# Kernel tuning notes

Measured on AMD Instinct MI355X. Metric: run time of the kernel, lower is better.

## Reference

```python
import jax, jax.numpy as jnp
import numpy as np

N_INP, N_INN, N_STEP = 512, 256, 3


def _linear(x, W, b):
    # torch nn.Linear convention: y = x @ W.T + b, W: (out, in)
    return x @ W.T + b


def _outer_linear(fv, W, b):
    # Linear(2h -> out) applied to outer_concat(fv) without materializing the 2h concat.
    # out[b,i,j] = fv[b,i] @ W[:, :h].T + fv[b,j] @ W[:, h:].T + b
    h = fv.shape[-1]
    x = fv @ W[:, :h].T  # (b, l, out)
    y = fv @ W[:, h:].T  # (b, l, out)
    return x[:, :, None, :] + y[:, None, :, :] + b  # (b, l, l, out)


def setup_inputs() -> dict:
    key = jax.random.key(0)
    ks = jax.random.split(key, 16)
    b, l = 8, 128
    s_inp = 1.0 / np.sqrt(N_INP)
    s_inn = 1.0 / np.sqrt(N_INN)
    s_2in = 1.0 / np.sqrt(2 * N_INN)
    u = lambda k, shape, s: jax.random.uniform(k, shape, jnp.float32, -s, s)
    return {
        "feat": jax.random.normal(ks[0], (b, l, N_INP), jnp.float32),
        "mask": jnp.ones((b, l), jnp.float32),
        "W_inp": u(ks[1], (N_INN, N_INP), s_inp), "b_inp": u(ks[2], (N_INN,), s_inp),
        "W_oup": u(ks[3], (N_INP, N_INN), s_inn), "b_oup": u(ks[4], (N_INP,), s_inn),
        "W_fe": u(ks[5], (N_INN, 2 * N_INN), s_2in), "b_fe": u(ks[6], (N_INN,), s_2in),
        "W_ue": u(ks[7], (N_INN, 2 * N_INN), s_2in), "b_ue": u(ks[8], (N_INN,), s_2in),
        "W_agg": u(ks[9], (N_INN, N_INN), s_inn), "b_agg": u(ks[10], (N_INN,), s_inn),
        "W_uv": u(ks[11], (N_INN, 2 * N_INN), s_2in), "b_uv": u(ks[12], (N_INN,), s_2in),
        "W_attn": u(ks[13], (N_INN, N_INN), s_inn), "b_attn": u(ks[14], (N_INN,), s_inn),
    }


def reference(feat, mask, W_inp, b_inp, W_oup, b_oup, W_fe, b_fe, W_ue, b_ue,
              W_agg, b_agg, W_uv, b_uv, W_attn, b_attn):
    h = N_INN
    fv = _linear(feat, W_inp, b_inp)                 # (b, l, h)
    fe = _outer_linear(fv, W_fe, b_fe)               # (b, l, l, h)
    for _ in range(N_STEP):
        # edge_update: xform_feat_e(outer_concat(fv)) then upd_e(concat(., fe))
        new_e = _outer_linear(fv, W_fe, b_fe)        # (b, l, l, h)
        fe = new_e @ W_ue[:, :h].T + fe @ W_ue[:, h:].T + b_ue
        # vertex_update (vectorized over j; softmax over source index i = dim 1)
        hid = fv * mask[:, :, None]
        xhid = _linear(hid, W_agg, b_agg)            # (b, l, h)
        attn = _linear(fe, W_attn, b_attn)           # (b, i, j, h)
        w = jax.nn.softmax(attn, axis=1)             # softmax over i
        agg = jax.nn.sigmoid(jnp.einsum('bijh,bih->bjh', w, xhid))  # (b, l, h)
        fv = _linear(jnp.concatenate([xhid, agg], axis=2), W_uv, b_uv)  # dropout = identity (eval)
    return _linear(fv, W_oup, b_oup)                 # (b, l, n_inp)
```

## Files before the change

kernel.cpp:

```cpp
#include <hip/hip_runtime.h>
#include <math.h>


typedef float f32x4  __attribute__((ext_vector_type(4)));
typedef short bf16x8 __attribute__((ext_vector_type(8)));

#define H  256
#define H2 512

__device__ __forceinline__ ushort f2bf(float f) {
    uint u = __float_as_uint(f);
    u += 0x7FFFu + ((u >> 16) & 1u);
    return (ushort)(u >> 16);
}
__device__ __forceinline__ float bf2f(ushort h) {
    return __uint_as_float(((uint)h) << 16);
}

struct Args {
    const float *feat, *mask, *b_inp, *b_oup, *b_agg, *b_uv;
    const float *W_fe, *W_inp, *W_oup, *W_ue, *W_agg, *W_uv, *W_attn;
    float *out;
    float *Wsa, *S, *Cb;
    ushort *featH,*featL, *WfeH,*WfeL, *WinpH,*WinpL, *WueH,*WueL,
           *WuvH,*WuvL, *WoupH,*WoupL, *WaggH,*WaggL,
           *WsaH,*WsaL, *WsabH,*WsabL, *WuebH,*WuebL,
           *fvH,*fvL, *fvmH,*fvmL, *xhH,*xhL, *p0H,*p0L, *p1H,*p1L;
};

struct Seg { const ushort *ah,*al,*bh,*bl; int lda, ldb, nk32; };

template<int MODE>
__device__ void wave_gemm32(const Seg* segs, int nseg,
                            float* yf, int ldy,
                            ushort* yh, ushort* yl, ushort* ymh, ushort* yml,
                            const float* bias, const float* cvec,
                            const float* mask, int bm, int bn, int lane)
{
    const int rl = lane & 15, kq = lane >> 4;
    f32x4 acc[2][2] = {};

    for (int s = 0; s < nseg; ++s) {
        const Seg sg = segs[s];
        for (int ks = 0; ks < sg.nk32; ++ks) {
            const int kb = ks * 32 + kq * 8;
            bf16x8 ah[2], al[2], bh[2], bl[2];
            #pragma unroll
            for (int mi = 0; mi < 2; ++mi) {
                const size_t ro = (size_t)(bm + mi * 16 + rl) * sg.lda + kb;
                ah[mi] = *(const bf16x8*)(sg.ah + ro);
                al[mi] = *(const bf16x8*)(sg.al + ro);
            }
            #pragma unroll
            for (int ni = 0; ni < 2; ++ni) {
                const size_t co = (size_t)(bn + ni * 16 + rl) * sg.ldb + kb;
                bh[ni] = *(const bf16x8*)(sg.bh + co);
                bl[ni] = *(const bf16x8*)(sg.bl + co);
            }
            #pragma unroll
            for (int mi = 0; mi < 2; ++mi)
                #pragma unroll
                for (int ni = 0; ni < 2; ++ni) {
                    acc[mi][ni] = __builtin_amdgcn_mfma_f32_16x16x32_bf16(
                        ah[mi], bh[ni], acc[mi][ni], 0, 0, 0);
                    acc[mi][ni] = __builtin_amdgcn_mfma_f32_16x16x32_bf16(
                        ah[mi], bl[ni], acc[mi][ni], 0, 0, 0);
                    acc[mi][ni] = __builtin_amdgcn_mfma_f32_16x16x32_bf16(
                        al[mi], bh[ni], acc[mi][ni], 0, 0, 0);
                }
        }
    }
    #pragma unroll
    for (int mi = 0; mi < 2; ++mi)
        #pragma unroll
        for (int ni = 0; ni < 2; ++ni) {
            const int col = bn + ni * 16 + rl;
            float bv = bias ? bias[col] : 0.f;
            if (MODE == 2 && cvec) bv += cvec[col];
            #pragma unroll
            for (int j = 0; j < 4; ++j) {
                const int row = bm + mi * 16 + kq * 4 + j;
                const float v = acc[mi][ni][j] + bv;
                if (MODE == 0) {
                    yf[(size_t)row * ldy + col] = v;
                } else {
                    const ushort hh = f2bf(v);
                    yh[(size_t)row * H + col] = hh;
                    yl[(size_t)row * H + col] = f2bf(v - bf2f(hh));
                    if (MODE == 2) {
                        const float mv = v * mask[row];
                        const ushort mh = f2bf(mv);
                        ymh[(size_t)row * H + col] = mh;
                        yml[(size_t)row * H + col] = f2bf(mv - bf2f(mh));
                    }
                }
            }
        }
}

__global__ __launch_bounds__(256) void k_prep(Args a)
{
    const int bid = blockIdx.x, tid = threadIdx.x;
    if (bid < 1024) {
        const float* src[7] = {a.feat, a.W_fe, a.W_inp, a.W_ue, a.W_uv,
                               a.W_oup, a.W_agg};
        ushort* dh[7] = {a.featH, a.WfeH, a.WinpH, a.WueH, a.WuvH,
                         a.WoupH, a.WaggH};
        ushort* dl[7] = {a.featL, a.WfeL, a.WinpL, a.WueL, a.WuvL,
                         a.WoupL, a.WaggL};
        const int n[7] = {524288, 131072, 131072, 131072, 131072, 131072, 65536};
        for (int e = 0; e < 7; ++e) {
            const float* sp = src[e];
            ushort *hp = dh[e], *lp = dl[e];
            for (int i = bid * 256 + tid; i < n[e]; i += 1024 * 256) {
                const float v = sp[i];
                const ushort hh = f2bf(v);
                hp[i] = hh;
                lp[i] = f2bf(v - bf2f(hh));
            }
        }
    } else {
        const int idx = (bid - 1024) * 256 + tid;
        const int i = idx >> 9, j = idx & 511;
        float acc = 0.f;
        const float* wa = a.W_attn + i * 256;
        const float* wu = a.W_ue + j;
        #pragma unroll 4
        for (int k = 0; k < 256; ++k)
            acc = fmaf(wa[k], wu[(size_t)k * 512], acc);
        a.Wsa[idx] = acc;
        const ushort hh = f2bf(acc);
        a.WsaH[idx] = hh;
        a.WsaL[idx] = f2bf(acc - bf2f(hh));
    }
}

__global__ __launch_bounds__(256) void k_folds(Args a)
{
    const int idx = blockIdx.x * 256 + threadIdx.x;
    const int which = idx >> 16;
    const int o = idx & 65535, i = o >> 8, j = o & 255;
    const float* xrow = (which == 0) ? (a.Wsa + i * 512) : (a.W_ue + i * 512);
    const float* wcol = a.W_fe + j;
    float acc = 0.f;
    #pragma unroll 4
    for (int k = 0; k < 256; ++k)
        acc = fmaf(xrow[k], wcol[(size_t)k * 512], acc);
    ushort* hp = (which == 0) ? a.WsabH : a.WuebH;
    ushort* lp = (which == 0) ? a.WsabL : a.WuebL;
    const ushort hh = f2bf(acc);
    hp[o] = hh;
    lp[o] = f2bf(acc - bf2f(hh));
}

__global__ __launch_bounds__(64) void k_fv0(Args a)
{
    const int bid = blockIdx.x;
    const int bm = (bid >> 3) << 5, bn = (bid & 7) << 5;
    Seg sg[1] = {{a.featH, a.featL, a.WinpH, a.WinpL, H2, H2, 16}};
    wave_gemm32<2>(sg, 1, nullptr, 0, a.fvH, a.fvL, a.fvmH, a.fvmL,
                   a.b_inp, nullptr, a.mask, bm, bn, threadIdx.x);
}

__global__ __launch_bounds__(64) void k_p0xh0(Args a)
{
    const int u = blockIdx.x, v = u & 255;
    const int bm = (v >> 3) << 5, bn = (v & 7) << 5;
    if (u < 256) {
        Seg sg[1] = {{a.fvH, a.fvL, a.WfeH, a.WfeL, H, H2, 8}};
        wave_gemm32<1>(sg, 1, nullptr, 0, a.p0H, a.p0L, nullptr, nullptr,
                       nullptr, nullptr, nullptr, bm, bn, threadIdx.x);
    } else {
        Seg sg[1] = {{a.fvmH, a.fvmL, a.WaggH, a.WaggL, H, H, 8}};
        wave_gemm32<1>(sg, 1, nullptr, 0, a.xhH, a.xhL, nullptr, nullptr,
                       a.b_agg, nullptr, nullptr, bm, bn, threadIdx.x);
    }
}

__global__ __launch_bounds__(64) void k_sph(Args a, int t)
{
    const int u = blockIdx.x, v = u & 255;
    const int bm = (v >> 3) << 5, bn = (v & 7) << 5;
    const ushort* pch = (t & 1) ? a.p1H : a.p0H;
    const ushort* pcl = (t & 1) ? a.p1L : a.p0L;
    ushort* pnh = (t & 1) ? a.p0H : a.p1H;
    ushort* pnl = (t & 1) ? a.p0L : a.p1L;
    const int which = (u < 256) ? 0 : (u < 512 ? (t < 2 ? 1 : 2) : 2);
    if (which == 0) {
        Seg sg[2] = {{a.fvH, a.fvL, a.WsabH, a.WsabL, H, H, 8},
                     {pch, pcl, a.WsaH + H, a.WsaL + H, H, H2, 8}};
        wave_gemm32<0>(sg, 2, a.S, H, nullptr, nullptr, nullptr, nullptr,
                       nullptr, nullptr, nullptr, bm, bn, threadIdx.x);
    } else if (which == 1) {
        Seg sg[2] = {{a.fvH, a.fvL, a.WuebH, a.WuebL, H, H, 8},
                     {pch, pcl, a.WueH + H, a.WueL + H, H, H2, 8}};
        wave_gemm32<1>(sg, 2, nullptr, 0, pnh, pnl, nullptr, nullptr,
                       nullptr, nullptr, nullptr, bm, bn, threadIdx.x);
    } else {
        Seg sg[1] = {{a.fvmH, a.fvmL, a.WaggH, a.WaggL, H, H, 8}};
        wave_gemm32<1>(sg, 1, nullptr, 0, a.xhH, a.xhL, nullptr, nullptr,
                       a.b_agg, nullptr, nullptr, bm, bn, threadIdx.x);
    }
}

__global__ __launch_bounds__(512) void k_sm(Args a)
{
    __shared__ float smem[2304];
    float* redm = smem;
    float* reds = smem + 512;
    float* reda = smem + 1024;
    float* aggv = smem + 1536;
    float* cpart = smem + 1792;
    const int b = blockIdx.x, tid = threadIdx.x;
    const int h = tid & 255, ig = tid >> 8;
    const int row0 = b * 128 + ig * 64;
    const float*  Sp = a.S + (size_t)row0 * H + h;
    const ushort* xh = a.xhH + (size_t)row0 * H + h;
    const ushort* xl = a.xhL + (size_t)row0 * H + h;

    float m = -3.402823466e38f, s = 0.f, acc = 0.f;
    for (int ii = 0; ii < 64; ++ii) {
        const float v = Sp[(size_t)ii * H];
        const float x = bf2f(xh[(size_t)ii * H]) + bf2f(xl[(size_t)ii * H]);
        const float nm = fmaxf(m, v);
        const float sc = __expf(m - nm);
        const float e  = __expf(v - nm);
        s = s * sc + e;
        acc = acc * sc + e * x;
        m = nm;
    }
    redm[ig * 256 + h] = m; reds[ig * 256 + h] = s; reda[ig * 256 + h] = acc;
    __syncthreads();
    {
        const float m0 = redm[h], m1 = redm[256 + h];
        const float M = fmaxf(m0, m1);
        const float S2 = reds[h] * __expf(m0 - M) + reds[256 + h] * __expf(m1 - M);
        const float A2 = reda[h] * __expf(m0 - M) + reda[256 + h] * __expf(m1 - M);
        const float g = 1.f / (1.f + __expf(-(A2 / S2)));
        if (ig == 0) aggv[h] = g;
    }
    __syncthreads();
    {
        const int n = tid >> 1, half = tid & 1;
        const ushort* wh = a.WuvH + (size_t)n * H2 + H + half * 128;
        const ushort* wl = a.WuvL + (size_t)n * H2 + H + half * 128;
        const float* av = aggv + half * 128;
        float c = 0.f;
        for (int q = 0; q < 16; ++q) {
            bf16x8 vh = *(const bf16x8*)(wh + q * 8);
            bf16x8 vl = *(const bf16x8*)(wl + q * 8);
            #pragma unroll
            for (int j = 0; j < 8; ++j)
                c += av[q * 8 + j] * (bf2f((ushort)vh[j]) + bf2f((ushort)vl[j]));
        }
        cpart[tid] = c;
    }
    __syncthreads();
    if (tid < 256) a.Cb[b * H + tid] = cpart[2 * tid] + cpart[2 * tid + 1];
}

__global__ __launch_bounds__(64) void k_fv(Args a)
{
    const int bid = blockIdx.x;
    const int bm = (bid >> 3) << 5, bn = (bid & 7) << 5;
    Seg sg[1] = {{a.xhH, a.xhL, a.WuvH, a.WuvL, H, H2, 8}};
    wave_gemm32<2>(sg, 1, nullptr, 0, a.fvH, a.fvL, a.fvmH, a.fvmL,
                   a.b_uv, a.Cb + (bm >> 7) * H, a.mask, bm, bn, threadIdx.x);
}

__global__ __launch_bounds__(64) void k_out(Args a)
{
    const int bid = blockIdx.x;
    const int bm = (bid >> 4) << 5, bn = (bid & 15) << 5;
    Seg sg[1] = {{a.fvH, a.fvL, a.WoupH, a.WoupL, H, H, 8}};
    wave_gemm32<0>(sg, 1, a.out, H2, nullptr, nullptr, nullptr, nullptr,
                   a.b_oup, nullptr, nullptr, bm, bn, threadIdx.x);
}

extern "C" void kernel_launch(void* const* d_in, const int* in_sizes, int n_in,
                              void* d_out, int out_size, void* d_ws, size_t ws_size,
                              hipStream_t stream)
{
    Args a;
    a.feat   = (const float*)d_in[0];
    a.mask   = (const float*)d_in[1];
    a.W_inp  = (const float*)d_in[2];
    a.b_inp  = (const float*)d_in[3];
    a.W_oup  = (const float*)d_in[4];
    a.b_oup  = (const float*)d_in[5];
    a.W_fe   = (const float*)d_in[6];
    a.W_ue   = (const float*)d_in[8];
    a.W_agg  = (const float*)d_in[10];
    a.b_agg  = (const float*)d_in[11];
    a.W_uv   = (const float*)d_in[12];
    a.b_uv   = (const float*)d_in[13];
    a.W_attn = (const float*)d_in[14];
    a.out    = (float*)d_out;

    float* fp = (float*)d_ws;
    a.Wsa = fp; fp += 131072;
    a.S   = fp; fp += 262144;
    a.Cb  = fp; fp += 2048;
    ushort* up = (ushort*)fp;
    auto take = [&](int n) { ushort* p = up; up += n; return p; };
    a.featH = take(524288); a.featL = take(524288);
    a.WfeH  = take(131072); a.WfeL  = take(131072);
    a.WinpH = take(131072); a.WinpL = take(131072);
    a.WueH  = take(131072); a.WueL  = take(131072);
    a.WuvH  = take(131072); a.WuvL  = take(131072);
    a.WoupH = take(131072); a.WoupL = take(131072);
    a.WaggH = take(65536);  a.WaggL = take(65536);
    a.WsaH  = take(131072); a.WsaL  = take(131072);
    a.WsabH = take(65536);  a.WsabL = take(65536);
    a.WuebH = take(65536);  a.WuebL = take(65536);
    a.fvH   = take(262144); a.fvL   = take(262144);
    a.fvmH  = take(262144); a.fvmL  = take(262144);
    a.xhH   = take(262144); a.xhL   = take(262144);
    a.p0H   = take(262144); a.p0L   = take(262144);
    a.p1H   = take(262144); a.p1L   = take(262144);

    k_prep <<<dim3(1536), dim3(256), 0, stream>>>(a);
    k_folds<<<dim3(512),  dim3(256), 0, stream>>>(a);
    k_fv0  <<<dim3(256),  dim3(64),  0, stream>>>(a);
    k_p0xh0<<<dim3(512),  dim3(64),  0, stream>>>(a);
    for (int t = 0; t < 3; ++t) {
        const int nblk = (t == 1) ? 768 : 512;
        k_sph<<<dim3(nblk), dim3(64),  0, stream>>>(a, t);
        k_sm <<<dim3(8),    dim3(512), 0, stream>>>(a);
        k_fv <<<dim3(256),  dim3(64),  0, stream>>>(a);
    }
    k_out  <<<dim3(512),  dim3(64),  0, stream>>>(a);
}
```

Baseline: 276.5 us.

## Fold vertex update weights algebraically and fuse each step into one kernel

Restructures the whole pipeline. Weight products (W_uv·W_agg, W_attn·W_ue·W_fe, W_oup·W_fv and others) are precomputed so the recurrence runs on the masked vertex features, with rank-one corrections carried by per-batch vectors from the sigmoid aggregate. Each step becomes a single kernel that does the GEMM tiles, softmax and aggregation in LDS, replacing the separate sph/sm/fv launches. It also drops the bf16 split conversion of feat and the full weight copies. This cuts launch count and global round trips, but the longer chains of folded products may change rounding, and the 64-block step kernels leave most of the GPU's compute units idle.

```diff
diff --git a/kernel.cpp b/kernel.cpp
--- a/kernel.cpp
+++ b/kernel.cpp
@@ -21,25 +21,89 @@
     const float *feat, *mask, *b_inp, *b_oup, *b_agg, *b_uv;
     const float *W_fe, *W_inp, *W_oup, *W_ue, *W_agg, *W_uv, *W_attn;
     float *out;
-    float *Wsa, *S, *Cb;
-    ushort *featH,*featL, *WfeH,*WfeL, *WinpH,*WinpL, *WueH,*WueL,
-           *WuvH,*WuvL, *WoupH,*WoupL, *WaggH,*WaggL,
-           *WsaH,*WsaL, *WsabH,*WsabL, *WuebH,*WuebL,
-           *fvH,*fvL, *fvmH,*fvmL, *xhH,*xhL, *p0H,*p0L, *p1H,*p1L;
+    float *Wsa1f, *Wsumf, *Wfvf, *Wsabf, *Wuebf, *vb0, *aggA, *aggB;
+    ushort *fv0H,*fv0L, *fvm0H,*fvm0L, *fvm1H,*fvm1L, *fvm2H,*fvm2L,
+           *p1H,*p1L, *p2H,*p2L,
+           *Wsa2H,*Wsa2L, *WfvH,*WfvL, *WagPH,*WagPL, *Wue2H,*Wue2L,
+           *Wsab2H,*Wsab2L, *Wueb2H,*Wueb2L, *WaggWfvH,*WaggWfvL,
+           *WsabWfvH,*WsabWfvL, *WuebWfvH,*WuebWfvL, *WoupWfvH,*WoupWfvL;
 };
 
+__device__ void f32core(const float* __restrict__ A, int lda, int aoff,
+                        const float* __restrict__ B, int ldb, int BT,
+                        int K, int bi, int bj, int tid, float* lds, float acc[4])
+{
+    float* Xt = lds;
+    float* Wt = lds + 1152;
+    const int lr = tid >> 3, lc = (tid & 7) << 2;
+    const int ty = tid >> 4, tx = tid & 15;
+    acc[0] = acc[1] = acc[2] = acc[3] = 0.f;
+    for (int k0 = 0; k0 < K; k0 += 32) {
+        const float* ap = A + (size_t)(bi + lr) * lda + k0 + lc;
+        float4 xv = *(const float4*)ap;
+        if (aoff) {
+            float4 x2 = *(const float4*)(ap + aoff);
+            xv.x += x2.x; xv.y += x2.y; xv.z += x2.z; xv.w += x2.w;
+        }
+        float4 wv;
+        if (BT) wv = *(const float4*)(B + (size_t)(bj + lr) * ldb + k0 + lc);
+        else    wv = *(const float4*)(B + (size_t)(k0 + lr) * ldb + bj + lc);
+        __syncthreads();
+        Xt[(lc+0)*36+lr] = xv.x; Xt[(lc+1)*36+lr] = xv.y;
+        Xt[(lc+2)*36+lr] = xv.z; Xt[(lc+3)*36+lr] = xv.w;
+        if (BT) {
+            Wt[(lc+0)*36+lr] = wv.x; Wt[(lc+1)*36+lr] = wv.y;
+            Wt[(lc+2)*36+lr] = wv.z; Wt[(lc+3)*36+lr] = wv.w;
+        } else {
+            *(float4*)(Wt + lr*36 + lc) = wv;
+        }
+        __syncthreads();
+        #pragma unroll
+        for (int kk = 0; kk < 32; ++kk) {
+            float2 x2 = *(const float2*)(Xt + kk*36 + 2*ty);
+            float2 w2 = *(const float2*)(Wt + kk*36 + 2*tx);
+            acc[0] = fmaf(x2.x, w2.x, acc[0]);
+            acc[1] = fmaf(x2.x, w2.y, acc[1]);
+            acc[2] = fmaf(x2.y, w2.x, acc[2]);
+            acc[3] = fmaf(x2.y, w2.y, acc[3]);
+        }
+    }
+}
+
+__device__ __forceinline__ void ep_planes(ushort* yh, ushort* yl, int ld,
+                                          int bi, int bj, int tid,
+                                          const float acc[4])
+{
+    const int ty = tid >> 4, tx = tid & 15;
+    #pragma unroll
+    for (int dy = 0; dy < 2; ++dy)
+        #pragma unroll
+        for (int dx = 0; dx < 2; ++dx) {
+            const int r = bi + 2*ty + dy, c = bj + 2*tx + dx;
+            const float v = acc[2*dy + dx];
+            const ushort hh = f2bf(v);
+            yh[(size_t)r*ld + c] = hh;
+            yl[(size_t)r*ld + c] = f2bf(v - bf2f(hh));
+        }
+}
+
 struct Seg { const ushort *ah,*al,*bh,*bl; int lda, ldb, nk32; };
+#define M_S   0
+#define M_XH  1
+#define M_P   2
+#define M_FVM 3
+#define M_OUT 4
 
 template<int MODE>
-__device__ void wave_gemm32(const Seg* segs, int nseg,
-                            float* yf, int ldy,
-                            ushort* yh, ushort* yl, ushort* ymh, ushort* yml,
-                            const float* bias, const float* cvec,
-                            const float* mask, int bm, int bn, int lane)
+__device__ void wtile(const Seg* segs, int nseg, int grow, int gcol,
+                      ushort* yh, ushort* yl, int ldy,
+                      float* ldsOut,
+                      float* yf, int ldyf,
+                      const float* vec, const float* bagg, const float* mask,
+                      int lane)
 {
     const int rl = lane & 15, kq = lane >> 4;
     f32x4 acc[2][2] = {};
-
     for (int s = 0; s < nseg; ++s) {
         const Seg sg = segs[s];
         for (int ks = 0; ks < sg.nk32; ++ks) {
@@ -47,13 +111,13 @@
             bf16x8 ah[2], al[2], bh[2], bl[2];
             #pragma unroll
             for (int mi = 0; mi < 2; ++mi) {
-                const size_t ro = (size_t)(bm + mi * 16 + rl) * sg.lda + kb;
+                const size_t ro = (size_t)(grow + mi*16 + rl) * sg.lda + kb;
                 ah[mi] = *(const bf16x8*)(sg.ah + ro);
                 al[mi] = *(const bf16x8*)(sg.al + ro);
             }
             #pragma unroll
             for (int ni = 0; ni < 2; ++ni) {
-                const size_t co = (size_t)(bn + ni * 16 + rl) * sg.ldb + kb;
+                const size_t co = (size_t)(gcol + ni*16 + rl) * sg.ldb + kb;
                 bh[ni] = *(const bf16x8*)(sg.bh + co);
                 bl[ni] = *(const bf16x8*)(sg.bl + co);
             }
@@ -74,25 +138,25 @@
     for (int mi = 0; mi < 2; ++mi)
         #pragma unroll
         for (int ni = 0; ni < 2; ++ni) {
-            const int col = bn + ni * 16 + rl;
-            float bv = bias ? bias[col] : 0.f;
-            if (MODE == 2 && cvec) bv += cvec[col];
+            const int lc = ni*16 + rl;
             #pragma unroll
             for (int j = 0; j < 4; ++j) {
-                const int row = bm + mi * 16 + kq * 4 + j;
-                const float v = acc[mi][ni][j] + bv;
-                if (MODE == 0) {
-                    yf[(size_t)row * ldy + col] = v;
+                const int lr = mi*16 + kq*4 + j;
+                float v = acc[mi][ni][j];
+                if (vec) v += vec[lc];
+                if (MODE == M_S) {
+                    ldsOut[lr*33 + lc] = v;
+                } else if (MODE == M_XH) {
+                    if (mask) v *= mask[grow + lr];
+                    v += bagg[gcol + lc];
+                    ldsOut[lr*33 + lc] = v;
+                } else if (MODE == M_P || MODE == M_FVM) {
+                    if (MODE == M_FVM) v *= mask[grow + lr];
+                    const ushort hh = f2bf(v);
+                    yh[(size_t)(grow+lr)*ldy + gcol + lc] = hh;
+                    yl[(size_t)(grow+lr)*ldy + gcol + lc] = f2bf(v - bf2f(hh));
                 } else {
-                    const ushort hh = f2bf(v);
-                    yh[(size_t)row * H + col] = hh;
-                    yl[(size_t)row * H + col] = f2bf(v - bf2f(hh));
-                    if (MODE == 2) {
-                        const float mv = v * mask[row];
-                        const ushort mh = f2bf(mv);
-                        ymh[(size_t)row * H + col] = mh;
-                        yml[(size_t)row * H + col] = f2bf(mv - bf2f(mh));
-                    }
+                    yf[(size_t)(grow+lr)*ldyf + gcol + lc] = v;
                 }
             }
         }
@@ -100,181 +164,290 @@
 
 __global__ __launch_bounds__(256) void k_prep(Args a)
 {
+    __shared__ float lds[2304];
+    const int u = blockIdx.x, tid = threadIdx.x;
+    float acc[4];
+    if (u < 256) {
+        const int bi = (u>>3)<<5, bj = (u&7)<<5;
+        f32core(a.feat, 512, 0, a.W_inp, 512, 1, 512, bi, bj, tid, lds, acc);
+        const int ty = tid>>4, tx = tid&15;
+        #pragma unroll
+        for (int dy = 0; dy < 2; ++dy)
+            #pragma unroll
+            for (int dx = 0; dx < 2; ++dx) {
+                const int r = bi + 2*ty + dy, c = bj + 2*tx + dx;
+                const float v = acc[2*dy+dx] + a.b_inp[c];
+                ushort hh = f2bf(v);
+                a.fv0H[r*H + c] = hh;
+                a.fv0L[r*H + c] = f2bf(v - bf2f(hh));
+                const float vm = v * a.mask[r];
+                hh = f2bf(vm);
+                a.fvm0H[r*H + c] = hh;
+                a.fvm0L[r*H + c] = f2bf(vm - bf2f(hh));
+            }
+    } else if (u < 320) {
+        const int v = u - 256;
+        const int bi = (v>>3)<<5, bj = (v&7)<<5;
+        float a2[4];
+        f32core(a.W_attn, 256, 0, a.W_ue,       512, 0, 256, bi, bj, tid, lds, acc);
+        f32core(a.W_attn, 256, 0, a.W_ue + 256, 512, 0, 256, bi, bj, tid, lds, a2);
+        const int ty = tid>>4, tx = tid&15;
+        #pragma unroll
+        for (int dy = 0; dy < 2; ++dy)
+            #pragma unroll
+            for (int dx = 0; dx < 2; ++dx) {
+                const int r = bi + 2*ty + dy, c = bj + 2*tx + dx;
+                const float v1 = acc[2*dy+dx], v2 = a2[2*dy+dx];
+                a.Wsa1f[r*H + c] = v1;
+                a.Wsumf[r*H + c] = v1 + v2;
+                const ushort hh = f2bf(v2);
+                a.Wsa2H[r*H + c] = hh;
+                a.Wsa2L[r*H + c] = f2bf(v2 - bf2f(hh));
+            }
+    } else if (u < 384) {
+        const int v = u - 320;
+        const int bi = (v>>3)<<5, bj = (v&7)<<5;
+        f32core(a.W_uv, 512, 0, a.W_agg, 256, 0, 256, bi, bj, tid, lds, acc);
+        const int ty = tid>>4, tx = tid&15;
+        #pragma unroll
+        for (int dy = 0; dy < 2; ++dy)
+            #pragma unroll
+            for (int dx = 0; dx < 2; ++dx) {
+                const int r = bi + 2*ty + dy, c = bj + 2*tx + dx;
+                const float v1 = acc[2*dy+dx];
+                a.Wfvf[r*H + c] = v1;
+                const ushort hh = f2bf(v1);
+                a.WfvH[r*H + c] = hh;
+                a.WfvL[r*H + c] = f2bf(v1 - bf2f(hh));
+            }
+    } else {
+        const int g = (u - 384) * 256 + tid;
+        #pragma unroll
+        for (int q = 0; q < 4; ++q) {
+            const int o = g*4 + q;
+            float v1 = a.W_agg[o];
+            ushort hh = f2bf(v1);
+            a.WagPH[o] = hh; a.WagPL[o] = f2bf(v1 - bf2f(hh));
+            const int n = o >> 8, k = o & 255;
+            const float v2 = a.W_ue[n*512 + 256 + k];
+            hh = f2bf(v2);
+            a.Wue2H[o] = hh; a.Wue2L[o] = f2bf(v2 - bf2f(hh));
+        }
+        if (g < 256) {
+            float s = a.b_uv[g];
+            const float* wr = a.W_uv + (size_t)g * 512;
+            for (int m = 0; m < 256; ++m) s = fmaf(wr[m], a.b_agg[m], s);
+            a.vb0[g] = s;
+        }
+    }
+}
+
+__global__ __launch_bounds__(256) void k_folds(Args a)
+{
+    __shared__ float lds[2304];
+    const int u = blockIdx.x, tid = threadIdx.x;
+    float acc[4];
+    const int ty = tid>>4, tx = tid&15;
+    if (u < 64) {
+        const int bi = (u>>3)<<5, bj = (u&7)<<5;
+        f32core(a.Wsa1f, 256, 0, a.W_fe, 512, 0, 256, bi, bj, tid, lds, acc);
+        #pragma unroll
+        for (int dy = 0; dy < 2; ++dy)
+            #pragma unroll
+            for (int dx = 0; dx < 2; ++dx)
+                a.Wsabf[(bi+2*ty+dy)*H + bj+2*tx+dx] = acc[2*dy+dx];
+    } else if (u < 128) {
+        const int v = u-64, bi = (v>>3)<<5, bj = (v&7)<<5;
+        f32core(a.W_ue, 512, 0, a.W_fe, 512, 0, 256, bi, bj, tid, lds, acc);
+        #pragma unroll
+        for (int dy = 0; dy < 2; ++dy)
+            #pragma unroll
+            for (int dx = 0; dx < 2; ++dx)
+                a.Wuebf[(bi+2*ty+dy)*H + bj+2*tx+dx] = acc[2*dy+dx];
+    } else if (u < 192) {
+        const int v = u-128, bi = (v>>3)<<5, bj = (v&7)<<5;
+        f32core(a.Wsumf, 256, 0, a.W_fe, 512, 0, 256, bi, bj, tid, lds, acc);
+        ep_planes(a.Wsab2H, a.Wsab2L, H, bi, bj, tid, acc);
+    } else if (u < 256) {
+        const int v = u-192, bi = (v>>3)<<5, bj = (v&7)<<5;
+        f32core(a.W_ue, 512, 256, a.W_fe, 512, 0, 256, bi, bj, tid, lds, acc);
+        ep_planes(a.Wueb2H, a.Wueb2L, H, bi, bj, tid, acc);
+    } else if (u < 320) {
+        const int v = u-256, bi = (v>>3)<<5, bj = (v&7)<<5;
+        f32core(a.W_agg, 256, 0, a.Wfvf, 256, 0, 256, bi, bj, tid, lds, acc);
+        ep_planes(a.WaggWfvH, a.WaggWfvL, H, bi, bj, tid, acc);
+    } else {
+        const int v = u-320, bi = (v>>3)<<5, bj = (v&7)<<5;
+        f32core(a.W_oup, 256, 0, a.Wfvf, 256, 0, 256, bi, bj, tid, lds, acc);
+        ep_planes(a.WoupWfvH, a.WoupWfvL, H, bi, bj, tid, acc);
+    }
+}
+
+__global__ __launch_bounds__(256) void k_step(Args a, int step)
+{
+    __shared__ float lds[9664];
     const int bid = blockIdx.x, tid = threadIdx.x;
-    if (bid < 1024) {
-        const float* src[7] = {a.feat, a.W_fe, a.W_inp, a.W_ue, a.W_uv,
-                               a.W_oup, a.W_agg};
-        ushort* dh[7] = {a.featH, a.WfeH, a.WinpH, a.WueH, a.WuvH,
-                         a.WoupH, a.WaggH};
-        ushort* dl[7] = {a.featL, a.WfeL, a.WinpL, a.WueL, a.WuvL,
-                         a.WoupL, a.WaggL};
-        const int n[7] = {524288, 131072, 131072, 131072, 131072, 131072, 65536};
-        for (int e = 0; e < 7; ++e) {
-            const float* sp = src[e];
-            ushort *hp = dh[e], *lp = dl[e];
-            for (int i = bid * 256 + tid; i < n[e]; i += 1024 * 256) {
-                const float v = sp[i];
-                const ushort hh = f2bf(v);
-                hp[i] = hh;
-                lp[i] = f2bf(v - bf2f(hh));
-            }
-        }
+
+    if (bid >= 64) {
+        int v = bid - 64;
+        float acc[4];
+        if (v < 64) {
+            const int bi = (v>>3)<<5, bj = (v&7)<<5;
+            f32core(a.Wsabf, 256, 0, a.Wfvf, 256, 0, 256, bi, bj, tid, lds, acc);
+            ep_planes(a.WsabWfvH, a.WsabWfvL, H, bi, bj, tid, acc);
+        } else {
+            v -= 64;
+            const int bi = (v>>3)<<5, bj = (v&7)<<5;
+            f32core(a.Wuebf, 256, 0, a.Wfvf, 256, 0, 256, bi, bj, tid, lds, acc);
+            ep_planes(a.WuebWfvH, a.WuebWfvL, H, bi, bj, tid, acc);
+        }
+        return;
+    }
+
+    const int b = bid >> 3, hb = (bid & 7) << 5;
+    const int rowb = b << 7;
+    float* Sl  = lds;
+    float* Xl  = lds + 4224;
+    float* dV  = lds + 8448;
+    float* sv  = lds + 8704;
+    float* pv  = lds + 8736;
+    float* xv  = lds + 8768;
+    float* fvv = lds + 8800;
+    float* red = lds + 8832;
+    float* Mv  = lds + 9600;
+
+    const float* aggIn  = (step == 2) ? a.aggB : a.aggA;
+    float*       aggOut = (step == 1) ? a.aggB : a.aggA;
+
+    if (step >= 1) {
+        float dd = a.vb0[tid];
+        const float* ag = aggIn + b * 256;
+        const float* wr = a.W_uv + (size_t)tid * 512 + 256;
+        for (int h = 0; h < 256; ++h) dd = fmaf(ag[h], wr[h], dd);
+        dV[tid] = dd;
+        __syncthreads();
+        if (tid < 32) {
+            float s = 0.f; const float* w = a.Wsabf + (size_t)(hb+tid)*H;
+            for (int k = 0; k < 256; ++k) s = fmaf(w[k], dV[k], s);
+            sv[tid] = s;
+        } else if (tid < 64) {
+            const int c = tid-32;
+            float s = 0.f; const float* w = a.Wuebf + (size_t)(hb+c)*H;
+            for (int k = 0; k < 256; ++k) s = fmaf(w[k], dV[k], s);
+            pv[c] = s;
+        } else if (tid < 96) {
+            const int c = tid-64;
+            float s = 0.f; const float* w = a.W_agg + (size_t)(hb+c)*H;
+            for (int k = 0; k < 256; ++k) s = fmaf(w[k], dV[k], s);
+            xv[c] = s;
+        } else if (tid < 128) {
+            fvv[tid-96] = dV[hb + tid-96];
+        }
+        __syncthreads();
+    }
+
+    const int lane = tid & 63, w = tid >> 6;
+    const int grow = rowb + w * 32;
+    float* SlW = Sl + w * 32 * 33;
+    float* XlW = Xl + w * 32 * 33;
+    Seg sg[2];
+
+    if (step == 0) {
+        sg[0] = {a.fv0H, a.fv0L, a.Wsab2H, a.Wsab2L, H, H, 8};
+        wtile<M_S>(sg, 1, grow, hb, nullptr, nullptr, 0, SlW,
+                   nullptr, 0, nullptr, nullptr, nullptr, lane);
+        sg[0] = {a.fvm0H, a.fvm0L, a.WagPH, a.WagPL, H, H, 8};
+        wtile<M_XH>(sg, 1, grow, hb, nullptr, nullptr, 0, XlW,
+                    nullptr, 0, nullptr, a.b_agg, nullptr, lane);
+        sg[0] = {a.fv0H, a.fv0L, a.Wueb2H, a.Wueb2L, H, H, 8};
+        wtile<M_P>(sg, 1, grow, hb, a.p1H, a.p1L, H, nullptr,
+                   nullptr, 0, nullptr, nullptr, nullptr, lane);
     } else {
-        const int idx = (bid - 1024) * 256 + tid;
-        const int i = idx >> 9, j = idx & 511;
-        float acc = 0.f;
-        const float* wa = a.W_attn + i * 256;
-        const float* wu = a.W_ue + j;
-        #pragma unroll 4
-        for (int k = 0; k < 256; ++k)
-            acc = fmaf(wa[k], wu[(size_t)k * 512], acc);
-        a.Wsa[idx] = acc;
-        const ushort hh = f2bf(acc);
-        a.WsaH[idx] = hh;
-        a.WsaL[idx] = f2bf(acc - bf2f(hh));
-    }
-}
-
-__global__ __launch_bounds__(256) void k_folds(Args a)
-{
-    const int idx = blockIdx.x * 256 + threadIdx.x;
-    const int which = idx >> 16;
-    const int o = idx & 65535, i = o >> 8, j = o & 255;
-    const float* xrow = (which == 0) ? (a.Wsa + i * 512) : (a.W_ue + i * 512);
-    const float* wcol = a.W_fe + j;
-    float acc = 0.f;
-    #pragma unroll 4
-    for (int k = 0; k < 256; ++k)
-        acc = fmaf(xrow[k], wcol[(size_t)k * 512], acc);
-    ushort* hp = (which == 0) ? a.WsabH : a.WuebH;
-    ushort* lp = (which == 0) ? a.WsabL : a.WuebL;
-    const ushort hh = f2bf(acc);
-    hp[o] = hh;
-    lp[o] = f2bf(acc - bf2f(hh));
-}
-
-__global__ __launch_bounds__(64) void k_fv0(Args a)
-{
-    const int bid = blockIdx.x;
-    const int bm = (bid >> 3) << 5, bn = (bid & 7) << 5;
-    Seg sg[1] = {{a.featH, a.featL, a.WinpH, a.WinpL, H2, H2, 16}};
-    wave_gemm32<2>(sg, 1, nullptr, 0, a.fvH, a.fvL, a.fvmH, a.fvmL,
-                   a.b_inp, nullptr, a.mask, bm, bn, threadIdx.x);
-}
-
-__global__ __launch_bounds__(64) void k_p0xh0(Args a)
-{
-    const int u = blockIdx.x, v = u & 255;
-    const int bm = (v >> 3) << 5, bn = (v & 7) << 5;
-    if (u < 256) {
-        Seg sg[1] = {{a.fvH, a.fvL, a.WfeH, a.WfeL, H, H2, 8}};
-        wave_gemm32<1>(sg, 1, nullptr, 0, a.p0H, a.p0L, nullptr, nullptr,
-                       nullptr, nullptr, nullptr, bm, bn, threadIdx.x);
-    } else {
-        Seg sg[1] = {{a.fvmH, a.fvmL, a.WaggH, a.WaggL, H, H, 8}};
-        wave_gemm32<1>(sg, 1, nullptr, 0, a.xhH, a.xhL, nullptr, nullptr,
-                       a.b_agg, nullptr, nullptr, bm, bn, threadIdx.x);
-    }
-}
-
-__global__ __launch_bounds__(64) void k_sph(Args a, int t)
-{
-    const int u = blockIdx.x, v = u & 255;
-    const int bm = (v >> 3) << 5, bn = (v & 7) << 5;
-    const ushort* pch = (t & 1) ? a.p1H : a.p0H;
-    const ushort* pcl = (t & 1) ? a.p1L : a.p0L;
-    ushort* pnh = (t & 1) ? a.p0H : a.p1H;
-    ushort* pnl = (t & 1) ? a.p0L : a.p1L;
-    const int which = (u < 256) ? 0 : (u < 512 ? (t < 2 ? 1 : 2) : 2);
-    if (which == 0) {
-        Seg sg[2] = {{a.fvH, a.fvL, a.WsabH, a.WsabL, H, H, 8},
-                     {pch, pcl, a.WsaH + H, a.WsaL + H, H, H2, 8}};
-        wave_gemm32<0>(sg, 2, a.S, H, nullptr, nullptr, nullptr, nullptr,
-                       nullptr, nullptr, nullptr, bm, bn, threadIdx.x);
-    } else if (which == 1) {
-        Seg sg[2] = {{a.fvH, a.fvL, a.WuebH, a.WuebL, H, H, 8},
-                     {pch, pcl, a.WueH + H, a.WueL + H, H, H2, 8}};
-        wave_gemm32<1>(sg, 2, nullptr, 0, pnh, pnl, nullptr, nullptr,
-                       nullptr, nullptr, nullptr, bm, bn, threadIdx.x);
-    } else {
-        Seg sg[1] = {{a.fvmH, a.fvmL, a.WaggH, a.WaggL, H, H, 8}};
-        wave_gemm32<1>(sg, 1, nullptr, 0, a.xhH, a.xhL, nullptr, nullptr,
-                       a.b_agg, nullptr, nullptr, bm, bn, threadIdx.x);
-    }
-}
-
-__global__ __launch_bounds__(512) void k_sm(Args a)
-{
-    __shared__ float smem[2304];
-    float* redm = smem;
-    float* reds = smem + 512;
-    float* reda = smem + 1024;
-    float* aggv = smem + 1536;
-    float* cpart = smem + 1792;
-    const int b = blockIdx.x, tid = threadIdx.x;
-    const int h = tid & 255, ig = tid >> 8;
-    const int row0 = b * 128 + ig * 64;
-    const float*  Sp = a.S + (size_t)row0 * H + h;
-    const ushort* xh = a.xhH + (size_t)row0 * H + h;
-    const ushort* xl = a.xhL + (size_t)row0 * H + h;
-
-    float m = -3.402823466e38f, s = 0.f, acc = 0.f;
-    for (int ii = 0; ii < 64; ++ii) {
-        const float v = Sp[(size_t)ii * H];
-        const float x = bf2f(xh[(size_t)ii * H]) + bf2f(xl[(size_t)ii * H]);
-        const float nm = fmaxf(m, v);
-        const float sc = __expf(m - nm);
-        const float e  = __expf(v - nm);
-        s = s * sc + e;
-        acc = acc * sc + e * x;
-        m = nm;
-    }
-    redm[ig * 256 + h] = m; reds[ig * 256 + h] = s; reda[ig * 256 + h] = acc;
+        const ushort* fh = (step == 1) ? a.fvm0H : a.fvm1H;
+        const ushort* fl = (step == 1) ? a.fvm0L : a.fvm1L;
+        const ushort* ph = (step == 1) ? a.p1H : a.p2H;
+        const ushort* pl = (step == 1) ? a.p1L : a.p2L;
+        ushort* nfh = (step == 1) ? a.fvm1H : a.fvm2H;
+        ushort* nfl = (step == 1) ? a.fvm1L : a.fvm2L;
+        sg[0] = {fh, fl, a.WfvH, a.WfvL, H, H, 8};
+        wtile<M_FVM>(sg, 1, grow, hb, nfh, nfl, H, nullptr,
+                     nullptr, 0, fvv, nullptr, a.mask, lane);
+        sg[0] = {fh, fl, a.WsabWfvH, a.WsabWfvL, H, H, 8};
+        sg[1] = {ph, pl, a.Wsa2H, a.Wsa2L, H, H, 8};
+        wtile<M_S>(sg, 2, grow, hb, nullptr, nullptr, 0, SlW,
+                   nullptr, 0, sv, nullptr, nullptr, lane);
+        sg[0] = {fh, fl, a.WaggWfvH, a.WaggWfvL, H, H, 8};
+        wtile<M_XH>(sg, 1, grow, hb, nullptr, nullptr, 0, XlW,
+                    nullptr, 0, xv, a.b_agg, a.mask, lane);
+        if (step == 1) {
+            sg[0] = {fh, fl, a.WuebWfvH, a.WuebWfvL, H, H, 8};
+            sg[1] = {ph, pl, a.Wue2H, a.Wue2L, H, H, 8};
+            wtile<M_P>(sg, 2, grow, hb, a.p2H, a.p2L, H, nullptr,
+                       nullptr, 0, pv, nullptr, nullptr, lane);
+        }
+    }
     __syncthreads();
-    {
-        const float m0 = redm[h], m1 = redm[256 + h];
-        const float M = fmaxf(m0, m1);
-        const float S2 = reds[h] * __expf(m0 - M) + reds[256 + h] * __expf(m1 - M);
-        const float A2 = reda[h] * __expf(m0 - M) + reda[256 + h] * __expf(m1 - M);
-        const float g = 1.f / (1.f + __expf(-(A2 / S2)));
-        if (ig == 0) aggv[h] = g;
-    }
+
+    const int c = tid & 31, g = tid >> 5;
+    float m = -3.402823466e38f;
+    #pragma unroll
+    for (int r = 0; r < 16; ++r)
+        m = fmaxf(m, Sl[(g*16 + r)*33 + c]);
+    red[g*32 + c] = m;
     __syncthreads();
-    {
-        const int n = tid >> 1, half = tid & 1;
-        const ushort* wh = a.WuvH + (size_t)n * H2 + H + half * 128;
-        const ushort* wl = a.WuvL + (size_t)n * H2 + H + half * 128;
-        const float* av = aggv + half * 128;
-        float c = 0.f;
-        for (int q = 0; q < 16; ++q) {
-            bf16x8 vh = *(const bf16x8*)(wh + q * 8);
-            bf16x8 vl = *(const bf16x8*)(wl + q * 8);
-            #pragma unroll
-            for (int j = 0; j < 8; ++j)
-                c += av[q * 8 + j] * (bf2f((ushort)vh[j]) + bf2f((ushort)vl[j]));
-        }
-        cpart[tid] = c;
+    if (g == 0) {
+        float M = red[c];
+        #pragma unroll
+        for (int q = 1; q < 8; ++q) M = fmaxf(M, red[q*32 + c]);
+        Mv[c] = M;
     }
     __syncthreads();
-    if (tid < 256) a.Cb[b * H + tid] = cpart[2 * tid] + cpart[2 * tid + 1];
-}
-
-__global__ __launch_bounds__(64) void k_fv(Args a)
-{
-    const int bid = blockIdx.x;
-    const int bm = (bid >> 3) << 5, bn = (bid & 7) << 5;
-    Seg sg[1] = {{a.xhH, a.xhL, a.WuvH, a.WuvL, H, H2, 8}};
-    wave_gemm32<2>(sg, 1, nullptr, 0, a.fvH, a.fvL, a.fvmH, a.fvmL,
-                   a.b_uv, a.Cb + (bm >> 7) * H, a.mask, bm, bn, threadIdx.x);
-}
-
-__global__ __launch_bounds__(64) void k_out(Args a)
-{
-    const int bid = blockIdx.x;
-    const int bm = (bid >> 4) << 5, bn = (bid & 15) << 5;
-    Seg sg[1] = {{a.fvH, a.fvL, a.WoupH, a.WoupL, H, H, 8}};
-    wave_gemm32<0>(sg, 1, a.out, H2, nullptr, nullptr, nullptr, nullptr,
-                   a.b_oup, nullptr, nullptr, bm, bn, threadIdx.x);
+    const float M = Mv[c];
+    float s = 0.f, ac = 0.f;
+    #pragma unroll
+    for (int r = 0; r < 16; ++r) {
+        const int rr = (g*16 + r)*33 + c;
+        const float e = __expf(Sl[rr] - M);
+        s += e;
+        ac = fmaf(e, Xl[rr], ac);
+    }
+    red[256 + g*32 + c] = s;
+    red[512 + g*32 + c] = ac;
+    __syncthreads();
+    if (g == 0) {
+        float S = 0.f, A = 0.f;
+        #pragma unroll
+        for (int q = 0; q < 8; ++q) {
+            S += red[256 + q*32 + c];
+            A += red[512 + q*32 + c];
+        }
+        aggOut[b*256 + hb + c] = 1.f / (1.f + __expf(-(A / S)));
+    }
+}
+
+__global__ __launch_bounds__(256) void k_out(Args a)
+{
+    __shared__ float lds[304];
+    float* d2 = lds; float* ov = lds + 256;
+    const int b = blockIdx.x >> 4, nb = (blockIdx.x & 15) << 5;
+    const int tid = threadIdx.x;
+    float dd = a.vb0[tid];
+    const float* ag = a.aggA + b * 256;
+    const float* wr = a.W_uv + (size_t)tid * 512 + 256;
+    for (int h = 0; h < 256; ++h) dd = fmaf(ag[h], wr[h], dd);
+    d2[tid] = dd;
+    __syncthreads();
+    if (tid < 32) {
+        float o = a.b_oup[nb + tid];
+        const float* wo = a.W_oup + (size_t)(nb + tid) * 256;
+        for (int k = 0; k < 256; ++k) o = fmaf(wo[k], d2[k], o);
+        ov[tid] = o;
+    }
+    __syncthreads();
+    const int lane = tid & 63, w = tid >> 6;
+    Seg sg[1] = {{a.fvm2H, a.fvm2L, a.WoupWfvH, a.WoupWfvL, H, H, 8}};
+    wtile<M_OUT>(sg, 1, b*128 + w*32, nb, nullptr, nullptr, 0, nullptr,
+                 a.out, H2, ov, nullptr, nullptr, lane);
 }
 
 extern "C" void kernel_launch(void* const* d_in, const int* in_sizes, int n_in,
@@ -298,36 +471,33 @@
     a.out    = (float*)d_out;
 
     float* fp = (float*)d_ws;
-    a.Wsa = fp; fp += 131072;
-    a.S   = fp; fp += 262144;
-    a.Cb  = fp; fp += 2048;
+    auto takef = [&](int n) { float* p = fp; fp += n; return p; };
+    a.Wsa1f = takef(65536); a.Wsumf = takef(65536); a.Wfvf = takef(65536);
+    a.Wsabf = takef(65536); a.Wuebf = takef(65536);
+    a.vb0 = takef(256); a.aggA = takef(2048); a.aggB = takef(2048);
     ushort* up = (ushort*)fp;
     auto take = [&](int n) { ushort* p = up; up += n; return p; };
-    a.featH = take(524288); a.featL = take(524288);
-    a.WfeH  = take(131072); a.WfeL  = take(131072);
-    a.WinpH = take(131072); a.WinpL = take(131072);
-    a.WueH  = take(131072); a.WueL  = take(131072);
-    a.WuvH  = take(131072); a.WuvL  = take(131072);
-    a.WoupH = take(131072); a.WoupL = take(131072);
-    a.WaggH = take(65536);  a.WaggL = take(65536);
-    a.WsaH  = take(131072); a.WsaL  = take(131072);
-    a.WsabH = take(65536);  a.WsabL = take(65536);
-    a.WuebH = take(65536);  a.WuebL = take(65536);
-    a.fvH   = take(262144); a.fvL   = take(262144);
-    a.fvmH  = take(262144); a.fvmL  = take(262144);
-    a.xhH   = take(262144); a.xhL   = take(262144);
-    a.p0H   = take(262144); a.p0L   = take(262144);
+    a.fv0H  = take(262144); a.fv0L  = take(262144);
+    a.fvm0H = take(262144); a.fvm0L = take(262144);
+    a.fvm1H = take(262144); a.fvm1L = take(262144);
+    a.fvm2H = take(262144); a.fvm2L = take(262144);
     a.p1H   = take(262144); a.p1L   = take(262144);
-
-    k_prep <<<dim3(1536), dim3(256), 0, stream>>>(a);
-    k_folds<<<dim3(512),  dim3(256), 0, stream>>>(a);
-    k_fv0  <<<dim3(256),  dim3(64),  0, stream>>>(a);
-    k_p0xh0<<<dim3(512),  dim3(64),  0, stream>>>(a);
-    for (int t = 0; t < 3; ++t) {
-        const int nblk = (t == 1) ? 768 : 512;
-        k_sph<<<dim3(nblk), dim3(64),  0, stream>>>(a, t);
-        k_sm <<<dim3(8),    dim3(512), 0, stream>>>(a);
-        k_fv <<<dim3(256),  dim3(64),  0, stream>>>(a);
-    }
-    k_out  <<<dim3(512),  dim3(64),  0, stream>>>(a);
-}
+    a.p2H   = take(262144); a.p2L   = take(262144);
+    a.Wsa2H = take(65536);  a.Wsa2L = take(65536);
+    a.WfvH  = take(65536);  a.WfvL  = take(65536);
+    a.WagPH = take(65536);  a.WagPL = take(65536);
+    a.Wue2H = take(65536);  a.Wue2L = take(65536);
+    a.Wsab2H = take(65536); a.Wsab2L = take(65536);
+    a.Wueb2H = take(65536); a.Wueb2L = take(65536);
+    a.WaggWfvH = take(65536); a.WaggWfvL = take(65536);
+    a.WsabWfvH = take(65536); a.WsabWfvL = take(65536);
+    a.WuebWfvH = take(65536); a.WuebWfvL = take(65536);
+    a.WoupWfvH = take(131072); a.WoupWfvL = take(131072);
+
+    k_prep <<<dim3(448), dim3(256), 0, stream>>>(a);
+    k_folds<<<dim3(448), dim3(256), 0, stream>>>(a);
+    k_step <<<dim3(192), dim3(256), 0, stream>>>(a, 0);
+    k_step <<<dim3(64),  dim3(256), 0, stream>>>(a, 1);
+    k_step <<<dim3(64),  dim3(256), 0, stream>>>(a, 2);
+    k_out  <<<dim3(128), dim3(256), 0, stream>>>(a);
+}
```

Result: no change. 276.7 us (+0.1%).
